# Kernel tuning notes

Measured on AMD Instinct MI355X. Metric: run time of the kernel, lower is better.

The kernel has to match this reference:

```python
import jax, jax.numpy as jnp
import numpy as np

N_RELS = 3
MAX_COMPS = 128
EMBED_DIM = 256
BATCH = 64
SEQ_LEN = 2048


def setup_inputs() -> dict:
    key = jax.random.key(0)
    k1, k2, k3 = jax.random.split(key, 3)
    embds = jax.random.normal(k1, (BATCH, SEQ_LEN, EMBED_DIM), dtype=jnp.float32)
    # sparse component-selection mask; p=0.04 -> ~82 components/sample (< MAX_COMPS-1)
    choice_mask = jax.random.bernoulli(k2, 0.04, (BATCH, SEQ_LEN)).astype(jnp.int32)
    # hk.Linear(n_rels*embed_dim, with_bias=False): W [embed_dim, n_rels*embed_dim]
    W = jax.random.normal(k3, (EMBED_DIM, N_RELS * EMBED_DIM), dtype=jnp.float32) / np.sqrt(EMBED_DIM).astype(np.float32)
    return {"embds": embds, "choice_mask": choice_mask, "W": W}


def _single(embds, mask, W):
    """One sample: gather selected embeddings, pad, project, pairwise relation scores.
    embds: [S, D], mask: [S] int, W: [D, D*R]. Returns [M, M, R]."""
    M, D, R = MAX_COMPS, EMBED_DIM, N_RELS
    # stable sort moves selected positions to the front, preserving order
    order = jnp.argsort(-mask)                      # [S]
    gathered = embds[order[: M - 1]]                # [M-1, D]
    n = jnp.minimum(jnp.sum(mask), M - 1)           # number of real components
    valid = jnp.arange(M - 1) < n                   # [M-1]
    comps = jnp.where(valid[:, None], gathered, jnp.zeros((), embds.dtype))
    # root component = row of ones (pad constant_values=1 at the front in the original)
    from_embds = jnp.concatenate([jnp.ones((1, D), embds.dtype), comps], axis=0)  # [M, D]
    to_embds = (from_embds @ W).reshape(M, D, R)    # [M, D, R]
    # jnp.dot([M,D], [M,D,R]) contracts D -> [M, M, R]
    log_energies = jnp.einsum('id,jdr->ijr', from_embds, to_embds)
    # no links FROM the root component (index 0)
    log_energies = log_energies.at[0].set(-jnp.inf)
    pad_mask = jnp.concatenate([jnp.ones((1,), bool), valid])   # [M]
    available = pad_mask[:, None] & pad_mask[None, :]           # [M, M]
    return jnp.where(available[:, :, None], log_energies, -jnp.inf)


def reference(embds, choice_mask, W):
    return jax.vmap(lambda e, m: _single(e, m, W))(embds, choice_mask)
```

## Files before the change

### kernel.cpp

```cpp
#include <hip/hip_runtime.h>
#include <math.h>

#define BATCH 64
#define SEQ   2048
#define DIM   256
#define NREL  3
#define MC    128
#define MV    127
#define NCOL  (DIM*NREL)
#define OUTC  (MC*NREL)

#define NEG_SENTINEL (-3.0e38f)

typedef __attribute__((ext_vector_type(8))) short short8;
typedef __attribute__((ext_vector_type(4))) float floatx4;
typedef __attribute__((ext_vector_type(4))) unsigned short us4;
typedef __attribute__((ext_vector_type(8))) unsigned short us8;

__device__ __forceinline__ unsigned short f2bf(float f) {
  unsigned int u = __builtin_bit_cast(unsigned int, f);
  unsigned int r = u + 0x7FFFu + ((u >> 16) & 1u);
  return (unsigned short)(r >> 16);
}

__global__ __launch_bounds__(256) void k_prep(const int* __restrict__ mask,
                                              const float* __restrict__ embds,
                                              unsigned short* __restrict__ fwb,
                                              int* __restrict__ n_ws) {
  int b = blockIdx.x, t = threadIdx.x;
  int lane = t & 63, wv = t >> 6;
  __shared__ int sel[MV];
  __shared__ int wsum[4];
  const int* m = mask + (size_t)b * SEQ;
  int base = t * 8;
  int vals[8];
  int c = 0;
#pragma unroll
  for (int k = 0; k < 8; k++) { vals[k] = m[base + k]; c += (vals[k] != 0); }
  int inc = c;
#pragma unroll
  for (int off = 1; off < 64; off <<= 1) {
    int o = __shfl_up(inc, off, 64);
    if (lane >= off) inc += o;
  }
  if (lane == 63) wsum[wv] = inc;
  __syncthreads();
  int wbase = 0;
#pragma unroll
  for (int w = 0; w < 4; w++) if (w < wv) wbase += wsum[w];
  int total = wsum[0] + wsum[1] + wsum[2] + wsum[3];
  int excl = wbase + inc - c;
  int rank = excl;
#pragma unroll
  for (int k = 0; k < 8; k++) {
    if (vals[k]) { if (rank < MV) sel[rank] = base + k; rank++; }
  }
  int n = (total < MV) ? total : MV;
  if (t == 0) n_ws[b] = n;
  __syncthreads();
  int lane16 = t & 15;
#pragma unroll
  for (int p = 0; p < 8; p++) {
    int i = p * 16 + (t >> 4);
    float f[16];
    if (i == 0) {
#pragma unroll
      for (int e = 0; e < 16; e++) f[e] = 1.f;
    } else if (i - 1 < n) {
      const float* src = embds + ((size_t)b * SEQ + sel[i - 1]) * DIM + lane16 * 16;
#pragma unroll
      for (int q = 0; q < 4; q++) *(float4*)&f[q * 4] = *(const float4*)(src + q * 4);
    } else {
#pragma unroll
      for (int e = 0; e < 16; e++) f[e] = 0.f;
    }
    us8 o0, o1;
#pragma unroll
    for (int e = 0; e < 8; e++) { o0[e] = f2bf(f[e]); o1[e] = f2bf(f[8 + e]); }
    unsigned short* dst = fwb + ((size_t)b * MC + i) * DIM + lane16 * 16;
    *(us8*)(dst) = o0;
    *(us8*)(dst + 8) = o1;
  }
}

__global__ __launch_bounds__(256) void k_wconv(const float* __restrict__ W,
                                               unsigned short* __restrict__ Wt) {
  int idx = blockIdx.x * 256 + threadIdx.x;
  int nn = idx >> 3;
  int k0 = (idx & 7) * 32;
  unsigned short tmp[32];
#pragma unroll
  for (int e = 0; e < 32; e++) tmp[e] = f2bf(W[(size_t)(k0 + e) * NCOL + nn]);
#pragma unroll
  for (int q = 0; q < 4; q++)
    *(us8*)(Wt + (size_t)nn * DIM + k0 + q * 8) = *(us8*)&tmp[q * 8];
}

__global__ __launch_bounds__(256) void k_gemm1(const unsigned short* __restrict__ fwb,
                                               const unsigned short* __restrict__ Wt,
                                               unsigned short* __restrict__ to_b) {
  int b = blockIdx.y;
  int n0 = blockIdx.x * 128;
  const unsigned short* A = fwb + (size_t)b * MC * DIM;
  int t = threadIdx.x;
  int wave = t >> 6, l = t & 63;
  int wr = wave >> 1, wc = wave & 1;
  int lm = l & 15, lk = (l >> 4) * 8;
  floatx4 acc[4][4] = {};
#pragma unroll 2
  for (int k0 = 0; k0 < DIM; k0 += 32) {
    short8 af[4], bf[4];
#pragma unroll
    for (int mi = 0; mi < 4; mi++)
      af[mi] = *(const short8*)(A + (size_t)(wr * 64 + mi * 16 + lm) * DIM + k0 + lk);
#pragma unroll
    for (int ni = 0; ni < 4; ni++)
      bf[ni] = *(const short8*)(Wt + (size_t)(n0 + wc * 64 + ni * 16 + lm) * DIM + k0 + lk);
#pragma unroll
    for (int mi = 0; mi < 4; mi++)
#pragma unroll
      for (int ni = 0; ni < 4; ni++)
        acc[mi][ni] = __builtin_amdgcn_mfma_f32_16x16x32_bf16(af[mi], bf[ni], acc[mi][ni], 0, 0, 0);
  }
  int rb = (l >> 4) * 4;
#pragma unroll
  for (int mi = 0; mi < 4; mi++)
#pragma unroll
    for (int ni = 0; ni < 4; ni++) {
      int ng = n0 + wc * 64 + ni * 16 + lm;
#pragma unroll
      for (int reg = 0; reg < 4; reg++) {
        int j = wr * 64 + mi * 16 + rb + reg;
        to_b[(size_t)b * MC * NCOL + (size_t)j * NCOL + ng] = f2bf(acc[mi][ni][reg]);
      }
    }
}

#define LDB 264
__global__ __launch_bounds__(256) void k_rel(const unsigned short* __restrict__ fwb,
                                             const unsigned short* __restrict__ to_b,
                                             const int* __restrict__ n_ws,
                                             float* __restrict__ out) {
  int b = blockIdx.y;
  int bc = blockIdx.x;
  int j0 = bc * 32, c0 = bc * 96;
  const unsigned short* A = fwb + (size_t)b * MC * DIM;
  const unsigned short* T = to_b + (size_t)b * MC * NCOL;
  __shared__ unsigned short Bs[96 * LDB];
  int t = threadIdx.x;
  int w = t >> 6, l = t & 63;
  int lm = l & 15, lk = (l >> 4) * 8;
  int jl = t >> 3;
  int l8 = t & 7;
#pragma unroll
  for (int ch = 0; ch < 8; ch++) {
    const unsigned short* src = T + (size_t)(j0 + jl) * NCOL + ch * 96 + l8 * 12;
    us4 q0 = *(const us4*)(src);
    us4 q1 = *(const us4*)(src + 4);
    us4 q2 = *(const us4*)(src + 8);
    unsigned short vv[12] = { q0.x, q0.y, q0.z, q0.w, q1.x, q1.y, q1.z, q1.w,
                              q2.x, q2.y, q2.z, q2.w };
#pragma unroll
    for (int e = 0; e < 12; e++) {
      int q = l8 * 12 + e;
      Bs[(jl * 3 + (q % 3)) * LDB + ch * 32 + (q / 3)] = vv[e];
    }
  }
  __syncthreads();
  floatx4 acc[2][6] = {};
#pragma unroll 2
  for (int k0 = 0; k0 < DIM; k0 += 32) {
    short8 af[2], bf[6];
#pragma unroll
    for (int mi = 0; mi < 2; mi++)
      af[mi] = *(const short8*)(A + (size_t)(w * 32 + mi * 16 + lm) * DIM + k0 + lk);
#pragma unroll
    for (int ci = 0; ci < 6; ci++)
      bf[ci] = *(const short8*)&Bs[(ci * 16 + lm) * LDB + k0 + lk];
#pragma unroll
    for (int mi = 0; mi < 2; mi++)
#pragma unroll
      for (int ci = 0; ci < 6; ci++)
        acc[mi][ci] = __builtin_amdgcn_mfma_f32_16x16x32_bf16(af[mi], bf[ci], acc[mi][ci], 0, 0, 0);
  }
  int n = n_ws[b];
  int rb = (l >> 4) * 4;
#pragma unroll
  for (int mi = 0; mi < 2; mi++)
#pragma unroll
    for (int ci = 0; ci < 6; ci++) {
      int cg = c0 + ci * 16 + lm;
      int j = cg / 3;
      bool vj = (j == 0) || (j <= n);
#pragma unroll
      for (int reg = 0; reg < 4; reg++) {
        int i = w * 32 + mi * 16 + rb + reg;
        bool vi = (i > 0) && (i <= n);
        out[(size_t)b * MC * OUTC + (size_t)i * OUTC + cg] =
            (vi && vj) ? acc[mi][ci][reg] : NEG_SENTINEL;
      }
    }
}

extern "C" void kernel_launch(void* const* d_in, const int* in_sizes, int n_in,
                              void* d_out, int out_size, void* d_ws, size_t ws_size,
                              hipStream_t stream) {
  const float* embds = (const float*)d_in[0];
  const int*   mask  = (const int*)d_in[1];
  const float* W     = (const float*)d_in[2];
  float* out = (float*)d_out;

  char* ws = (char*)d_ws;
  int* n_ws = (int*)(ws + 0);
  unsigned short* fwb  = (unsigned short*)(ws + 65536);
  unsigned short* Wt   = (unsigned short*)(ws + 65536 + 4*1024*1024);
  unsigned short* to_b = (unsigned short*)(ws + 65536 + 5*1024*1024);

  k_wconv<<<dim3(24),       dim3(256), 0, stream>>>(W, Wt);
  k_prep <<<dim3(BATCH),    dim3(256), 0, stream>>>(mask, embds, fwb, n_ws);
  k_gemm1<<<dim3(6, BATCH), dim3(256), 0, stream>>>(fwb, Wt, to_b);
  k_rel  <<<dim3(4, BATCH), dim3(256), 0, stream>>>(fwb, to_b, n_ws, out);
}
```

Before: 202.0 us.

## Fuse projection GEMM into relation kernel and merge weight conversion into prep

Folds the W bf16 conversion into the prep kernel as extra blocks. The per-sample projection GEMM now runs inside the relation kernel: each block computes its 32-row slice of from_embds@W directly into shared memory, already transposed into the layout the second GEMM needs. This drops two launches and the global round trip of the intermediate to_b tensor. In exchange each block does a 32x768x256 GEMM with 24 accumulators per thread, which raises register pressure, and it streams all of Wt from global or L2 per block.

New measurement: 199.3 us. About the same (-1.3%).

```diff
diff --git a/kernel.cpp b/kernel.cpp
--- a/kernel.cpp
+++ b/kernel.cpp
@@ -14,7 +14,6 @@
 
 typedef __attribute__((ext_vector_type(8))) short short8;
 typedef __attribute__((ext_vector_type(4))) float floatx4;
-typedef __attribute__((ext_vector_type(4))) unsigned short us4;
 typedef __attribute__((ext_vector_type(8))) unsigned short us8;
 
 __device__ __forceinline__ unsigned short f2bf(float f) {
@@ -25,9 +24,24 @@
 
 __global__ __launch_bounds__(256) void k_prep(const int* __restrict__ mask,
                                               const float* __restrict__ embds,
+                                              const float* __restrict__ W,
                                               unsigned short* __restrict__ fwb,
+                                              unsigned short* __restrict__ Wt,
                                               int* __restrict__ n_ws) {
-  int b = blockIdx.x, t = threadIdx.x;
+  int t = threadIdx.x;
+  if (blockIdx.x < 24) {
+    int idx = blockIdx.x * 256 + t;
+    int nn = idx >> 3;
+    int k0 = (idx & 7) * 32;
+    unsigned short tmp[32];
+#pragma unroll
+    for (int e = 0; e < 32; e++) tmp[e] = f2bf(W[(size_t)(k0 + e) * NCOL + nn]);
+#pragma unroll
+    for (int q = 0; q < 4; q++)
+      *(us8*)(Wt + (size_t)nn * DIM + k0 + q * 8) = *(us8*)&tmp[q * 8];
+    return;
+  }
+  int b = blockIdx.x - 24;
   int lane = t & 63, wv = t >> 6;
   __shared__ int sel[MV];
   __shared__ int wsum[4];
@@ -49,8 +63,7 @@
 #pragma unroll
   for (int w = 0; w < 4; w++) if (w < wv) wbase += wsum[w];
   int total = wsum[0] + wsum[1] + wsum[2] + wsum[3];
-  int excl = wbase + inc - c;
-  int rank = excl;
+  int rank = wbase + inc - c;
 #pragma unroll
   for (int k = 0; k < 8; k++) {
     if (vals[k]) { if (rank < MV) sel[rank] = base + k; rank++; }
@@ -83,90 +96,47 @@
   }
 }
 
-__global__ __launch_bounds__(256) void k_wconv(const float* __restrict__ W,
-                                               unsigned short* __restrict__ Wt) {
-  int idx = blockIdx.x * 256 + threadIdx.x;
-  int nn = idx >> 3;
-  int k0 = (idx & 7) * 32;
-  unsigned short tmp[32];
-#pragma unroll
-  for (int e = 0; e < 32; e++) tmp[e] = f2bf(W[(size_t)(k0 + e) * NCOL + nn]);
-#pragma unroll
-  for (int q = 0; q < 4; q++)
-    *(us8*)(Wt + (size_t)nn * DIM + k0 + q * 8) = *(us8*)&tmp[q * 8];
-}
-
-__global__ __launch_bounds__(256) void k_gemm1(const unsigned short* __restrict__ fwb,
+#define LDB 264
+__global__ __launch_bounds__(256) void k_fused(const unsigned short* __restrict__ fwb,
                                                const unsigned short* __restrict__ Wt,
-                                               unsigned short* __restrict__ to_b) {
-  int b = blockIdx.y;
-  int n0 = blockIdx.x * 128;
-  const unsigned short* A = fwb + (size_t)b * MC * DIM;
-  int t = threadIdx.x;
-  int wave = t >> 6, l = t & 63;
-  int wr = wave >> 1, wc = wave & 1;
-  int lm = l & 15, lk = (l >> 4) * 8;
-  floatx4 acc[4][4] = {};
-#pragma unroll 2
-  for (int k0 = 0; k0 < DIM; k0 += 32) {
-    short8 af[4], bf[4];
-#pragma unroll
-    for (int mi = 0; mi < 4; mi++)
-      af[mi] = *(const short8*)(A + (size_t)(wr * 64 + mi * 16 + lm) * DIM + k0 + lk);
-#pragma unroll
-    for (int ni = 0; ni < 4; ni++)
-      bf[ni] = *(const short8*)(Wt + (size_t)(n0 + wc * 64 + ni * 16 + lm) * DIM + k0 + lk);
-#pragma unroll
-    for (int mi = 0; mi < 4; mi++)
-#pragma unroll
-      for (int ni = 0; ni < 4; ni++)
-        acc[mi][ni] = __builtin_amdgcn_mfma_f32_16x16x32_bf16(af[mi], bf[ni], acc[mi][ni], 0, 0, 0);
-  }
-  int rb = (l >> 4) * 4;
-#pragma unroll
-  for (int mi = 0; mi < 4; mi++)
-#pragma unroll
-    for (int ni = 0; ni < 4; ni++) {
-      int ng = n0 + wc * 64 + ni * 16 + lm;
-#pragma unroll
-      for (int reg = 0; reg < 4; reg++) {
-        int j = wr * 64 + mi * 16 + rb + reg;
-        to_b[(size_t)b * MC * NCOL + (size_t)j * NCOL + ng] = f2bf(acc[mi][ni][reg]);
-      }
-    }
-}
-
-#define LDB 264
-__global__ __launch_bounds__(256) void k_rel(const unsigned short* __restrict__ fwb,
-                                             const unsigned short* __restrict__ to_b,
-                                             const int* __restrict__ n_ws,
-                                             float* __restrict__ out) {
+                                               const int* __restrict__ n_ws,
+                                               float* __restrict__ out) {
   int b = blockIdx.y;
   int bc = blockIdx.x;
   int j0 = bc * 32, c0 = bc * 96;
   const unsigned short* A = fwb + (size_t)b * MC * DIM;
-  const unsigned short* T = to_b + (size_t)b * MC * NCOL;
   __shared__ unsigned short Bs[96 * LDB];
   int t = threadIdx.x;
   int w = t >> 6, l = t & 63;
-  int lm = l & 15, lk = (l >> 4) * 8;
-  int jl = t >> 3;
-  int l8 = t & 7;
+  int lm = l & 15, lk = (l >> 4) * 8, rb = (l >> 4) * 4;
+
+  floatx4 acc1[2][12] = {};
+#pragma unroll 2
+  for (int k0 = 0; k0 < DIM; k0 += 32) {
+    short8 af0 = *(const short8*)(A + (size_t)(j0 + lm) * DIM + k0 + lk);
+    short8 af1 = *(const short8*)(A + (size_t)(j0 + 16 + lm) * DIM + k0 + lk);
 #pragma unroll
-  for (int ch = 0; ch < 8; ch++) {
-    const unsigned short* src = T + (size_t)(j0 + jl) * NCOL + ch * 96 + l8 * 12;
-    us4 q0 = *(const us4*)(src);
-    us4 q1 = *(const us4*)(src + 4);
-    us4 q2 = *(const us4*)(src + 8);
-    unsigned short vv[12] = { q0.x, q0.y, q0.z, q0.w, q1.x, q1.y, q1.z, q1.w,
-                              q2.x, q2.y, q2.z, q2.w };
-#pragma unroll
-    for (int e = 0; e < 12; e++) {
-      int q = l8 * 12 + e;
-      Bs[(jl * 3 + (q % 3)) * LDB + ch * 32 + (q / 3)] = vv[e];
+    for (int ni = 0; ni < 12; ni++) {
+      int n = w * 192 + ni * 16 + lm;
+      short8 bf = *(const short8*)(Wt + (size_t)n * DIM + k0 + lk);
+      acc1[0][ni] = __builtin_amdgcn_mfma_f32_16x16x32_bf16(af0, bf, acc1[0][ni], 0, 0, 0);
+      acc1[1][ni] = __builtin_amdgcn_mfma_f32_16x16x32_bf16(af1, bf, acc1[1][ni], 0, 0, 0);
     }
   }
+#pragma unroll
+  for (int ni = 0; ni < 12; ni++) {
+    int n = w * 192 + ni * 16 + lm;
+    int dd = n / 3, r = n - dd * 3;
+#pragma unroll
+    for (int mi = 0; mi < 2; mi++)
+#pragma unroll
+      for (int reg = 0; reg < 4; reg++) {
+        int jl = mi * 16 + rb + reg;
+        Bs[(jl * 3 + r) * LDB + dd] = f2bf(acc1[mi][ni][reg]);
+      }
+  }
   __syncthreads();
+
   floatx4 acc[2][6] = {};
 #pragma unroll 2
   for (int k0 = 0; k0 < DIM; k0 += 32) {
@@ -184,7 +154,6 @@
         acc[mi][ci] = __builtin_amdgcn_mfma_f32_16x16x32_bf16(af[mi], bf[ci], acc[mi][ci], 0, 0, 0);
   }
   int n = n_ws[b];
-  int rb = (l >> 4) * 4;
 #pragma unroll
   for (int mi = 0; mi < 2; mi++)
 #pragma unroll
@@ -212,12 +181,9 @@
 
   char* ws = (char*)d_ws;
   int* n_ws = (int*)(ws + 0);
-  unsigned short* fwb  = (unsigned short*)(ws + 65536);
-  unsigned short* Wt   = (unsigned short*)(ws + 65536 + 4*1024*1024);
-  unsigned short* to_b = (unsigned short*)(ws + 65536 + 5*1024*1024);
+  unsigned short* fwb = (unsigned short*)(ws + 65536);
+  unsigned short* Wt  = (unsigned short*)(ws + 65536 + 4*1024*1024);
 
-  k_wconv<<<dim3(24),       dim3(256), 0, stream>>>(W, Wt);
-  k_prep <<<dim3(BATCH),    dim3(256), 0, stream>>>(mask, embds, fwb, n_ws);
-  k_gemm1<<<dim3(6, BATCH), dim3(256), 0, stream>>>(fwb, Wt, to_b);
-  k_rel  <<<dim3(4, BATCH), dim3(256), 0, stream>>>(fwb, to_b, n_ws, out);
+  k_prep <<<dim3(24 + BATCH), dim3(256), 0, stream>>>(mask, embds, W, fwb, Wt, n_ws);
+  k_fused<<<dim3(4, BATCH),   dim3(256), 0, stream>>>(fwb, Wt, n_ws, out);
 }
```
